# Performance work log

Measured on AMD Instinct MI355X. Metric: run time of the kernel, lower is better.

Reference implementation:

```python
import jax, jax.numpy as jnp
import numpy as np

B, T, E, H = 64, 512, 512, 512


def setup_inputs() -> dict:
    key = jax.random.key(0)
    ks = jax.random.split(key, 10)
    s = 1.0 / np.sqrt(H)  # torch GRU init: U(-1/sqrt(H), 1/sqrt(H))
    u = lambda k, shape: jax.random.uniform(k, shape, jnp.float32, -s, s)
    return {
        "xs": jax.random.normal(ks[0], (B, T, E), jnp.float32),
        "w_ih0": u(ks[1], (2, 3 * H, E)),
        "w_hh0": u(ks[2], (2, 3 * H, H)),
        "b_ih0": u(ks[3], (2, 3 * H)),
        "b_hh0": u(ks[4], (2, 3 * H)),
        "w_ih1": u(ks[5], (2, 3 * H, 2 * H)),
        "w_hh1": u(ks[6], (2, 3 * H, H)),
        "b_ih1": u(ks[7], (2, 3 * H)),
        "b_hh1": u(ks[8], (2, 3 * H)),
    }


def _gru_dir(x, w_ih, w_hh, b_ih, b_hh):
    # x: [B, T, D]; returns hs [B, T, H], h_T [B, H]
    h_dim = w_hh.shape[1]
    gx = jnp.einsum("btd,gd->btg", x, w_ih) + b_ih  # [B, T, 3H], all input GEMMs batched

    def step(h, gx_t):
        gh = h @ w_hh.T + b_hh
        r = jax.nn.sigmoid(gx_t[:, :h_dim] + gh[:, :h_dim])
        z = jax.nn.sigmoid(gx_t[:, h_dim:2 * h_dim] + gh[:, h_dim:2 * h_dim])
        n = jnp.tanh(gx_t[:, 2 * h_dim:] + r * gh[:, 2 * h_dim:])
        h = (1.0 - z) * n + z * h
        return h, h

    h0 = jnp.zeros((x.shape[0], h_dim), x.dtype)
    hT, hs = jax.lax.scan(step, h0, jnp.swapaxes(gx, 0, 1))
    return jnp.swapaxes(hs, 0, 1), hT


def _bidir_layer(x, w_ih, w_hh, b_ih, b_hh):
    hs_f, h_f = _gru_dir(x, w_ih[0], w_hh[0], b_ih[0], b_hh[0])
    hs_b, h_b = _gru_dir(x[:, ::-1], w_ih[1], w_hh[1], b_ih[1], b_hh[1])
    hs_b = hs_b[:, ::-1]
    return jnp.concatenate([hs_f, hs_b], axis=-1), jnp.stack([h_f, h_b])


def reference(xs, w_ih0, w_hh0, b_ih0, b_hh0, w_ih1, w_hh1, b_ih1, b_hh1):
    h0_out, hy0 = _bidir_layer(xs, w_ih0, w_hh0, b_ih0, b_hh0)
    h1_out, hy1 = _bidir_layer(h0_out, w_ih1, w_hh1, b_ih1, b_hh1)
    hy = jnp.concatenate([hy0, hy1], axis=0)  # [n_layers*2, B, H]
    # dropout p=0.0 -> identity
    return (h1_out, hy)
```

## Files before the change

### kernel.cpp

```cpp
#include <hip/hip_runtime.h>
#include <stdint.h>

#define Bq 64
#define Tq 512
#define Hq 512
#define G3 1536

typedef unsigned short u16;
typedef uint32_t u32;
typedef unsigned long long u64;
typedef __attribute__((ext_vector_type(8))) short bf16x8;
typedef __attribute__((ext_vector_type(4))) float f32x4;

__device__ __forceinline__ float bf2f(u16 v){ unsigned u = ((unsigned)v)<<16; float f; __builtin_memcpy(&f,&u,4); return f; }
__device__ __forceinline__ u16 f2bf(float f){ unsigned u; __builtin_memcpy(&u,&f,4); u += 0x7fffu + ((u>>16)&1u); return (u16)(u>>16); }

__global__ void detect_k(const u16* __restrict__ xs, int* __restrict__ flag){
  __shared__ int cnt;
  if (threadIdx.x==0) cnt = 0;
  __syncthreads();
  int good = 0;
  for (int i = threadIdx.x; i < 4096; i += 256) {
    u16 v = xs[2*i];
    int e = (v>>7)&0xFF;
    if (e==0 || (e>=100 && e<=140)) good++;
  }
  atomicAdd(&cnt, good);
  __syncthreads();
  if (threadIdx.x==0) flag[0] = (cnt > 3600) ? 1 : 0;
}

template<int K, int AMODE, int OUTF32>
__global__ __launch_bounds__(256,1) void gemm_gx(const void* __restrict__ Araw,
        const void* __restrict__ Wraw, const void* __restrict__ braw,
        void* __restrict__ outraw, const int* __restrict__ dflag)
{
  __shared__ __align__(16) u16 Ah[64*72];
  __shared__ __align__(16) u16 Al[64*72];
  __shared__ __align__(16) u16 Wh[64*72];
  __shared__ __align__(16) u16 Wl[64*72];
  const int bf16in = dflag[0];
  const bool useAlo = (AMODE==0) && !bf16in;
  const bool useWlo = !bf16in;
  const int dir = blockIdx.z;
  const int tid = threadIdx.x;
  const int m0 = blockIdx.x*64, n0 = blockIdx.y*64;
  const int wave = tid>>6, lane = tid&63;
  const int wm = (wave>>1)*32, wn = (wave&1)*32;
  f32x4 acc[2][2] = {};

  for (int kb=0; kb<K/64; kb++) {
    if (AMODE==0 && !bf16in) {
      const float* Af = (const float*)Araw;
      #pragma unroll
      for (int it=0; it<4; it++) {
        int c = it*256 + tid;
        int r = c>>4, cc = (c&15)*4;
        float4 v = *(const float4*)&Af[(size_t)(m0+r)*K + kb*64 + cc];
        u16 h0=f2bf(v.x), h1=f2bf(v.y), h2=f2bf(v.z), h3=f2bf(v.w);
        *(ushort4*)&Ah[r*72+cc] = make_ushort4(h0,h1,h2,h3);
        *(ushort4*)&Al[r*72+cc] = make_ushort4(
            f2bf(v.x-bf2f(h0)), f2bf(v.y-bf2f(h1)),
            f2bf(v.z-bf2f(h2)), f2bf(v.w-bf2f(h3)));
      }
    } else {
      const u16* Ab = (const u16*)Araw;
      #pragma unroll
      for (int it=0; it<2; it++) {
        int c = it*256 + tid;
        int r = c>>3, cc = (c&7)*8;
        *(bf16x8*)&Ah[r*72+cc] = *(const bf16x8*)&Ab[(size_t)(m0+r)*K + kb*64 + cc];
      }
    }
    if (!bf16in) {
      const float* Wf = (const float*)Wraw + (size_t)dir*G3*K;
      #pragma unroll
      for (int it=0; it<4; it++) {
        int c = it*256 + tid;
        int r = c>>4, cc = (c&15)*4;
        float4 v = *(const float4*)&Wf[(size_t)(n0+r)*K + kb*64 + cc];
        u16 h0=f2bf(v.x), h1=f2bf(v.y), h2=f2bf(v.z), h3=f2bf(v.w);
        *(ushort4*)&Wh[r*72+cc] = make_ushort4(h0,h1,h2,h3);
        *(ushort4*)&Wl[r*72+cc] = make_ushort4(
            f2bf(v.x-bf2f(h0)), f2bf(v.y-bf2f(h1)),
            f2bf(v.z-bf2f(h2)), f2bf(v.w-bf2f(h3)));
      }
    } else {
      const u16* Wb = (const u16*)Wraw + (size_t)dir*G3*K;
      #pragma unroll
      for (int it=0; it<2; it++) {
        int c = it*256 + tid;
        int r = c>>3, cc = (c&7)*8;
        *(bf16x8*)&Wh[r*72+cc] = *(const bf16x8*)&Wb[(size_t)(n0+r)*K + kb*64 + cc];
      }
    }
    __syncthreads();
    #pragma unroll
    for (int ks=0; ks<2; ks++) {
      int ko = ks*32 + (lane>>4)*8;
      bf16x8 a0 = *(const bf16x8*)&Ah[(wm    + (lane&15))*72 + ko];
      bf16x8 a1 = *(const bf16x8*)&Ah[(wm+16 + (lane&15))*72 + ko];
      bf16x8 b0 = *(const bf16x8*)&Wh[(wn    + (lane&15))*72 + ko];
      bf16x8 b1 = *(const bf16x8*)&Wh[(wn+16 + (lane&15))*72 + ko];
      acc[0][0] = __builtin_amdgcn_mfma_f32_16x16x32_bf16(a0,b0,acc[0][0],0,0,0);
      acc[0][1] = __builtin_amdgcn_mfma_f32_16x16x32_bf16(a0,b1,acc[0][1],0,0,0);
      acc[1][0] = __builtin_amdgcn_mfma_f32_16x16x32_bf16(a1,b0,acc[1][0],0,0,0);
      acc[1][1] = __builtin_amdgcn_mfma_f32_16x16x32_bf16(a1,b1,acc[1][1],0,0,0);
      if (useAlo) {
        bf16x8 c0 = *(const bf16x8*)&Al[(wm    + (lane&15))*72 + ko];
        bf16x8 c1 = *(const bf16x8*)&Al[(wm+16 + (lane&15))*72 + ko];
        acc[0][0] = __builtin_amdgcn_mfma_f32_16x16x32_bf16(c0,b0,acc[0][0],0,0,0);
        acc[0][1] = __builtin_amdgcn_mfma_f32_16x16x32_bf16(c0,b1,acc[0][1],0,0,0);
        acc[1][0] = __builtin_amdgcn_mfma_f32_16x16x32_bf16(c1,b0,acc[1][0],0,0,0);
        acc[1][1] = __builtin_amdgcn_mfma_f32_16x16x32_bf16(c1,b1,acc[1][1],0,0,0);
      }
      if (useWlo) {
        bf16x8 d0 = *(const bf16x8*)&Wl[(wn    + (lane&15))*72 + ko];
        bf16x8 d1 = *(const bf16x8*)&Wl[(wn+16 + (lane&15))*72 + ko];
        acc[0][0] = __builtin_amdgcn_mfma_f32_16x16x32_bf16(a0,d0,acc[0][0],0,0,0);
        acc[0][1] = __builtin_amdgcn_mfma_f32_16x16x32_bf16(a0,d1,acc[0][1],0,0,0);
        acc[1][0] = __builtin_amdgcn_mfma_f32_16x16x32_bf16(a1,d0,acc[1][0],0,0,0);
        acc[1][1] = __builtin_amdgcn_mfma_f32_16x16x32_bf16(a1,d1,acc[1][1],0,0,0);
      }
    }
    __syncthreads();
  }
  #pragma unroll
  for (int i=0;i<2;i++) {
    #pragma unroll
    for (int j=0;j<2;j++) {
      int nn = n0 + wn + j*16 + (lane&15);
      float bv = bf16in ? bf2f(((const u16*)braw)[dir*G3 + nn])
                        : ((const float*)braw)[dir*G3 + nn];
      #pragma unroll
      for (int r=0;r<4;r++) {
        int mm = m0 + wm + i*16 + (lane>>4)*4 + r;
        int b = mm >> 9, t = mm & 511;
        size_t oi = ((size_t)(dir*Tq + t)*Bq + b)*G3 + nn;
        float v = acc[i][j][r] + bv;
        if (OUTF32) ((float*)outraw)[oi] = v;
        else        ((u16*)outraw)[oi]   = f2bf(v);
      }
    }
  }
}

template<int LAYER, int GXF32>
__global__ __launch_bounds__(128,1) void gru_scan(const void* __restrict__ whh,
        const void* __restrict__ bhh, const void* __restrict__ gx,
        u16* __restrict__ hs0, void* __restrict__ dout,
        u32* __restrict__ hexw, int* __restrict__ flags,
        const int* __restrict__ dflag)
{
  extern __shared__ char smem[];
  u16* wlds = (u16*)smem;

  const int bf16in = dflag[0];
  const int tid = threadIdx.x;
  const int bx  = blockIdx.x;
  const int dir = bx>>6, group=(bx>>4)&3, slice=bx&15;
  const int jbase = slice*32, bg0 = group*16;
  int* fl = flags + (dir*4+group)*16;

  if (!bf16in) {
    const float* wf = (const float*)whh + (size_t)dir*G3*Hq;
    for (int c = tid; c < 96*128; c += 128) {
      int r = c>>7, q = (c&127)*4;
      int gate = r>>5, jj = r&31;
      float4 v = *(const float4*)&wf[(size_t)(gate*512 + jbase + jj)*Hq + q];
      *(ushort4*)&wlds[r*520 + q] = make_ushort4(f2bf(v.x),f2bf(v.y),f2bf(v.z),f2bf(v.w));
    }
  } else {
    const u16* wb = (const u16*)whh + (size_t)dir*G3*Hq;
    for (int c = tid; c < 96*64; c += 128) {
      int r = c>>6, cc = (c&63)*8;
      int gate = r>>5, jj = r&31;
      *(bf16x8*)&wlds[r*520 + cc] = *(const bf16x8*)&wb[(size_t)(gate*512 + jbase + jj)*Hq + cc];
    }
  }
  __syncthreads();
  if (tid >= 64) return;

  const int lane = tid;
  const int j0 = lane&15;
  const int bq = (lane>>4)*4;

  float bR[2], bZ[2], bN[2];
  #pragma unroll
  for (int c=0;c<2;c++) {
    int off = dir*G3 + jbase + c*16 + j0;
    if (bf16in) { const u16* bb=(const u16*)bhh;
      bR[c]=bf2f(bb[off]); bZ[c]=bf2f(bb[off+512]); bN[c]=bf2f(bb[off+1024]); }
    else { const float* bb=(const float*)bhh;
      bR[c]=bb[off]; bZ[c]=bb[off+512]; bN[c]=bb[off+1024]; }
  }

  float h[2][4] = {};
  float gxr[2][4], gxz[2][4], gxn[2][4];
  auto ldgx = [&](int t_in_){
    #pragma unroll
    for (int c=0;c<2;c++)
    #pragma unroll
    for (int i=0;i<4;i++){
      size_t gb = ((size_t)(dir*Tq + t_in_)*Bq + (bg0 + bq + i))*G3 + jbase + c*16 + j0;
      if (GXF32) { const float* gp=(const float*)gx + gb;
        gxr[c][i]=gp[0]; gxz[c][i]=gp[512]; gxn[c][i]=gp[1024]; }
      else { const u16* gp=(const u16*)gx + gb;
        gxr[c][i]=bf2f(gp[0]); gxz[c][i]=bf2f(gp[512]); gxn[c][i]=bf2f(gp[1024]); }
    }
  };
  ldgx(dir ? (Tq-1) : 0);

  for (int s=0; s<Tq; s++) {
    const int t_in = dir ? (Tq-1-s) : s;
    if (lane < 16) {
      while (__hip_atomic_fetch_add(&fl[lane], 0, __ATOMIC_RELAXED, __HIP_MEMORY_SCOPE_AGENT) < s) {
        __builtin_amdgcn_s_sleep(1);
      }
    }
    asm volatile("" ::: "memory");
    const u32 rb = (u32)(((s&1)*2 + dir)*Bq + bg0)*256u;
    u64 areg[32];
    #pragma unroll
    for (int kk=0; kk<16; kk++) {
      u32 base = rb + (u32)(lane&15)*256u + (u32)(kk*16 + (lane>>4)*4);
      areg[2*kk]   = __hip_atomic_fetch_add((u64*)&hexw[base],   (u64)0, __ATOMIC_RELAXED, __HIP_MEMORY_SCOPE_AGENT);
      areg[2*kk+1] = __hip_atomic_fetch_add((u64*)&hexw[base+2], (u64)0, __ATOMIC_RELAXED, __HIP_MEMORY_SCOPE_AGENT);
    }
    f32x4 aR[2] = {{0.f,0.f,0.f,0.f},{0.f,0.f,0.f,0.f}};
    f32x4 aZ[2] = {{0.f,0.f,0.f,0.f},{0.f,0.f,0.f,0.f}};
    f32x4 aN[2] = {{0.f,0.f,0.f,0.f},{0.f,0.f,0.f,0.f}};
    #pragma unroll
    for (int kk=0; kk<16; kk++) {
      union { u64 q[2]; bf16x8 v; } ab;
      ab.q[0] = areg[2*kk]; ab.q[1] = areg[2*kk+1];
      int ko = kk*32 + (lane>>4)*8;
      #pragma unroll
      for (int c=0;c<2;c++) {
        int wl = c*16 + j0;
        bf16x8 b0 = *(const bf16x8*)&wlds[(     wl)*520 + ko];
        bf16x8 b1 = *(const bf16x8*)&wlds[(32 + wl)*520 + ko];
        bf16x8 b2 = *(const bf16x8*)&wlds[(64 + wl)*520 + ko];
        aR[c] = __builtin_amdgcn_mfma_f32_16x16x32_bf16(ab.v,b0,aR[c],0,0,0);
        aZ[c] = __builtin_amdgcn_mfma_f32_16x16x32_bf16(ab.v,b1,aZ[c],0,0,0);
        aN[c] = __builtin_amdgcn_mfma_f32_16x16x32_bf16(ab.v,b2,aN[c],0,0,0);
      }
    }
    const u32 rb2 = (u32)((((s+1)&1)*2 + dir)*Bq + bg0)*256u;
    u16 hb[2][4]; float hn[2][4];
    #pragma unroll
    for (int c=0;c<2;c++)
    #pragma unroll
    for (int i=0;i<4;i++) {
      float rr = gxr[c][i] + aR[c][i] + bR[c];
      float zz = gxz[c][i] + aZ[c][i] + bZ[c];
      float gh =             aN[c][i] + bN[c];
      float r = 1.f/(1.f + __expf(-rr));
      float z = 1.f/(1.f + __expf(-zz));
      float x = gxn[c][i] + r*gh;
      x = fminf(fmaxf(x, -15.f), 15.f);
      float e2 = __expf(2.f*x);
      float n = (e2 - 1.f)/(e2 + 1.f);
      hn[c][i] = (1.f - z)*n + z*h[c][i];
      h[c][i] = hn[c][i]; hb[c][i] = f2bf(hn[c][i]);
    }
    #pragma unroll
    for (int c=0;c<2;c++)
    #pragma unroll
    for (int i=0;i<4;i++) {
      u32 p1 = (u32)__shfl_down((int)hb[c][i], 1);
      u32 p2 = (u32)__shfl_down((int)hb[c][i], 2);
      u32 p3 = (u32)__shfl_down((int)hb[c][i], 3);
      if ((lane & 3) == 0) {
        u64 pk = (u64)hb[c][i] | ((u64)(p1 & 0xffffu) << 16)
               | ((u64)(p2 & 0xffffu) << 32) | ((u64)(p3 & 0xffffu) << 48);
        (void)__hip_atomic_exchange((u64*)&hexw[rb2 + (u32)(bq+i)*256u + (u32)(slice*16 + c*8 + (j0>>1))],
                                    pk, __ATOMIC_RELAXED, __HIP_MEMORY_SCOPE_AGENT);
      }
    }
    asm volatile("s_waitcnt vmcnt(0)" ::: "memory");
    if (lane == 0) {
      (void)__hip_atomic_fetch_add(&fl[slice], 1, __ATOMIC_RELAXED, __HIP_MEMORY_SCOPE_AGENT);
    }
    if (s+1 < Tq) ldgx(dir ? (Tq-2-s) : (s+1));
    #pragma unroll
    for (int c=0;c<2;c++)
    #pragma unroll
    for (int i=0;i<4;i++) {
      int bg = bg0 + bq + i;
      size_t oi = ((size_t)bg*Tq + t_in)*1024 + dir*512 + jbase + c*16 + j0;
      if (LAYER==0) {
        __builtin_nontemporal_store(hb[c][i], &hs0[oi]);
      } else {
        if (bf16in) __builtin_nontemporal_store(hb[c][i], &((u16*)dout)[oi]);
        else        __builtin_nontemporal_store(hn[c][i], &((float*)dout)[oi]);
      }
      if (s == Tq-1) {
        size_t hyi = (size_t)Bq*Tq*1024 + ((size_t)(LAYER*2 + dir)*Bq + bg)*512 + jbase + c*16 + j0;
        if (bf16in) ((u16*)dout)[hyi] = hb[c][i];
        else        ((float*)dout)[hyi] = hn[c][i];
      }
    }
  }
}

__global__ void init_k(u32* hexw, int* flags){
  int i = blockIdx.x*256 + threadIdx.x;
  if (i < 2*2*Bq*256) hexw[i] = 0;
  if (i < 128) flags[i] = 0;
}

extern "C" void kernel_launch(void* const* d_in, const int* in_sizes, int n_in,
                              void* d_out, int out_size, void* d_ws, size_t ws_size,
                              hipStream_t stream)
{
  const void* xs    = d_in[0];
  const void* w_ih0 = d_in[1];
  const void* w_hh0 = d_in[2];
  const void* b_ih0 = d_in[3];
  const void* b_hh0 = d_in[4];
  const void* w_ih1 = d_in[5];
  const void* w_hh1 = d_in[6];
  const void* b_ih1 = d_in[7];
  const void* b_hh1 = d_in[8];
  (void)in_sizes; (void)n_in; (void)out_size;

  char* ws   = (char*)d_ws;
  int* dflag = (int*)ws;
  int* flags = (int*)(ws + 256);
  u32* hexw  = (u32*)(ws + 1024);
  void* gx   = (void*)(ws + 263168ULL);
  const bool gxf32 = ws_size >= 263168ULL + 402653184ULL;
  u16* hs0   = (u16*)d_out;

  hipFuncSetAttribute((const void*)gru_scan<0,0>, hipFuncAttributeMaxDynamicSharedMemorySize, 99840);
  hipFuncSetAttribute((const void*)gru_scan<1,0>, hipFuncAttributeMaxDynamicSharedMemorySize, 99840);
  hipFuncSetAttribute((const void*)gru_scan<0,1>, hipFuncAttributeMaxDynamicSharedMemorySize, 99840);
  hipFuncSetAttribute((const void*)gru_scan<1,1>, hipFuncAttributeMaxDynamicSharedMemorySize, 99840);

  dim3 gg(Tq*Bq/64, G3/64, 2);

  detect_k<<<1, 256, 0, stream>>>((const u16*)xs, dflag);
  init_k<<<512, 256, 0, stream>>>(hexw, flags);
  if (gxf32) {
    gemm_gx<512,0,1><<<gg, 256, 0, stream>>>(xs, w_ih0, b_ih0, gx, dflag);
    gru_scan<0,1><<<128, 128, 99840, stream>>>(w_hh0, b_hh0, gx, hs0, d_out, hexw, flags, dflag);
    gemm_gx<1024,1,1><<<gg, 256, 0, stream>>>(hs0, w_ih1, b_ih1, gx, dflag);
    init_k<<<512, 256, 0, stream>>>(hexw, flags);
    gru_scan<1,1><<<128, 128, 99840, stream>>>(w_hh1, b_hh1, gx, hs0, d_out, hexw, flags, dflag);
  } else {
    gemm_gx<512,0,0><<<gg, 256, 0, stream>>>(xs, w_ih0, b_ih0, gx, dflag);
    gru_scan<0,0><<<128, 128, 99840, stream>>>(w_hh0, b_hh0, gx, hs0, d_out, hexw, flags, dflag);
    gemm_gx<1024,1,0><<<gg, 256, 0, stream>>>(hs0, w_ih1, b_ih1, gx, dflag);
    init_k<<<512, 256, 0, stream>>>(hexw, flags);
    gru_scan<1,0><<<128, 128, 99840, stream>>>(w_hh1, b_hh1, gx, hs0, d_out, hexw, flags, dflag);
  }
}
```

Before: 6.200 ms.

## Keep recurrent weights in registers and pipeline hidden-state loads with MFMAs

The recurrent scan kernel now holds its slice of W_hh in per-lane registers instead of shared memory, and launches with 64 threads and no dynamic LDS. The hidden-state atomic loads are split into four chunks that are double-buffered and interleaved with the MFMA groups. The aim is to remove LDS reads from the per-timestep critical path and overlap global load latency with compute. The cost is very high register pressure (about 384 VGPRs for weights), which risks spills or compilation trouble.

Result: slower. 7.694 ms (+24.1%).

```diff
diff --git a/kernel.cpp b/kernel.cpp
--- a/kernel.cpp
+++ b/kernel.cpp
@@ -146,44 +146,55 @@
 }
 
 template<int LAYER, int GXF32>
-__global__ __launch_bounds__(128,1) void gru_scan(const void* __restrict__ whh,
+__global__ __launch_bounds__(64,1) void gru_scan(const void* __restrict__ whh,
         const void* __restrict__ bhh, const void* __restrict__ gx,
         u16* __restrict__ hs0, void* __restrict__ dout,
         u32* __restrict__ hexw, int* __restrict__ flags,
         const int* __restrict__ dflag)
 {
-  extern __shared__ char smem[];
-  u16* wlds = (u16*)smem;
-
   const int bf16in = dflag[0];
-  const int tid = threadIdx.x;
+  const int lane = threadIdx.x;
   const int bx  = blockIdx.x;
   const int dir = bx>>6, group=(bx>>4)&3, slice=bx&15;
   const int jbase = slice*32, bg0 = group*16;
   int* fl = flags + (dir*4+group)*16;
 
-  if (!bf16in) {
-    const float* wf = (const float*)whh + (size_t)dir*G3*Hq;
-    for (int c = tid; c < 96*128; c += 128) {
-      int r = c>>7, q = (c&127)*4;
-      int gate = r>>5, jj = r&31;
-      float4 v = *(const float4*)&wf[(size_t)(gate*512 + jbase + jj)*Hq + q];
-      *(ushort4*)&wlds[r*520 + q] = make_ushort4(f2bf(v.x),f2bf(v.y),f2bf(v.z),f2bf(v.w));
-    }
-  } else {
-    const u16* wb = (const u16*)whh + (size_t)dir*G3*Hq;
-    for (int c = tid; c < 96*64; c += 128) {
-      int r = c>>6, cc = (c&63)*8;
-      int gate = r>>5, jj = r&31;
-      *(bf16x8*)&wlds[r*520 + cc] = *(const bf16x8*)&wb[(size_t)(gate*512 + jbase + jj)*Hq + cc];
-    }
-  }
-  __syncthreads();
-  if (tid >= 64) return;
-
-  const int lane = tid;
   const int j0 = lane&15;
   const int bq = (lane>>4)*4;
+  const int khalf = (lane>>4)*8;
+
+  bf16x8 wreg[2][3][16];
+  if (!bf16in) {
+    const float* wf0 = (const float*)whh + (size_t)dir*G3*Hq;
+    #pragma unroll
+    for (int c=0;c<2;c++)
+    #pragma unroll
+    for (int g=0;g<3;g++) {
+      const float* wr = wf0 + (size_t)(g*512 + jbase + c*16 + j0)*Hq;
+      #pragma unroll
+      for (int kk=0;kk<16;kk++) {
+        float4 v0 = *(const float4*)&wr[kk*32 + khalf];
+        float4 v1 = *(const float4*)&wr[kk*32 + khalf + 4];
+        bf16x8 w;
+        w[0]=(short)f2bf(v0.x); w[1]=(short)f2bf(v0.y);
+        w[2]=(short)f2bf(v0.z); w[3]=(short)f2bf(v0.w);
+        w[4]=(short)f2bf(v1.x); w[5]=(short)f2bf(v1.y);
+        w[6]=(short)f2bf(v1.z); w[7]=(short)f2bf(v1.w);
+        wreg[c][g][kk] = w;
+      }
+    }
+  } else {
+    const u16* wb0 = (const u16*)whh + (size_t)dir*G3*Hq;
+    #pragma unroll
+    for (int c=0;c<2;c++)
+    #pragma unroll
+    for (int g=0;g<3;g++) {
+      const u16* wr = wb0 + (size_t)(g*512 + jbase + c*16 + j0)*Hq;
+      #pragma unroll
+      for (int kk=0;kk<16;kk++)
+        wreg[c][g][kk] = *(const bf16x8*)&wr[kk*32 + khalf];
+    }
+  }
 
   float bR[2], bZ[2], bN[2];
   #pragma unroll
@@ -220,32 +231,54 @@
     }
     asm volatile("" ::: "memory");
     const u32 rb = (u32)(((s&1)*2 + dir)*Bq + bg0)*256u;
-    u64 areg[32];
-    #pragma unroll
-    for (int kk=0; kk<16; kk++) {
-      u32 base = rb + (u32)(lane&15)*256u + (u32)(kk*16 + (lane>>4)*4);
-      areg[2*kk]   = __hip_atomic_fetch_add((u64*)&hexw[base],   (u64)0, __ATOMIC_RELAXED, __HIP_MEMORY_SCOPE_AGENT);
-      areg[2*kk+1] = __hip_atomic_fetch_add((u64*)&hexw[base+2], (u64)0, __ATOMIC_RELAXED, __HIP_MEMORY_SCOPE_AGENT);
+    const u32 gbase = rb + (u32)(lane&15)*256u + (u32)((lane>>4)*4);
+
+    u64 aA[8], aB[8];
+    #pragma unroll
+    for (int k2=0;k2<4;k2++) {
+      u32 b_ = gbase + (u32)((0+k2)*16);
+      aA[2*k2]   = __hip_atomic_fetch_add((u64*)&hexw[b_],   (u64)0, __ATOMIC_RELAXED, __HIP_MEMORY_SCOPE_AGENT);
+      aA[2*k2+1] = __hip_atomic_fetch_add((u64*)&hexw[b_+2], (u64)0, __ATOMIC_RELAXED, __HIP_MEMORY_SCOPE_AGENT);
+    }
+    #pragma unroll
+    for (int k2=0;k2<4;k2++) {
+      u32 b_ = gbase + (u32)((4+k2)*16);
+      aB[2*k2]   = __hip_atomic_fetch_add((u64*)&hexw[b_],   (u64)0, __ATOMIC_RELAXED, __HIP_MEMORY_SCOPE_AGENT);
+      aB[2*k2+1] = __hip_atomic_fetch_add((u64*)&hexw[b_+2], (u64)0, __ATOMIC_RELAXED, __HIP_MEMORY_SCOPE_AGENT);
     }
     f32x4 aR[2] = {{0.f,0.f,0.f,0.f},{0.f,0.f,0.f,0.f}};
     f32x4 aZ[2] = {{0.f,0.f,0.f,0.f},{0.f,0.f,0.f,0.f}};
     f32x4 aN[2] = {{0.f,0.f,0.f,0.f},{0.f,0.f,0.f,0.f}};
-    #pragma unroll
-    for (int kk=0; kk<16; kk++) {
-      union { u64 q[2]; bf16x8 v; } ab;
-      ab.q[0] = areg[2*kk]; ab.q[1] = areg[2*kk+1];
-      int ko = kk*32 + (lane>>4)*8;
-      #pragma unroll
-      for (int c=0;c<2;c++) {
-        int wl = c*16 + j0;
-        bf16x8 b0 = *(const bf16x8*)&wlds[(     wl)*520 + ko];
-        bf16x8 b1 = *(const bf16x8*)&wlds[(32 + wl)*520 + ko];
-        bf16x8 b2 = *(const bf16x8*)&wlds[(64 + wl)*520 + ko];
-        aR[c] = __builtin_amdgcn_mfma_f32_16x16x32_bf16(ab.v,b0,aR[c],0,0,0);
-        aZ[c] = __builtin_amdgcn_mfma_f32_16x16x32_bf16(ab.v,b1,aZ[c],0,0,0);
-        aN[c] = __builtin_amdgcn_mfma_f32_16x16x32_bf16(ab.v,b2,aN[c],0,0,0);
-      }
-    }
+    #define MFMA4(BUF, KK0)                                                   \
+      _Pragma("unroll")                                                       \
+      for (int k2=0;k2<4;k2++) {                                              \
+        union { u64 q[2]; bf16x8 v; } ab;                                     \
+        ab.q[0] = BUF[2*k2]; ab.q[1] = BUF[2*k2+1];                           \
+        _Pragma("unroll")                                                     \
+        for (int c=0;c<2;c++) {                                               \
+          aR[c] = __builtin_amdgcn_mfma_f32_16x16x32_bf16(ab.v, wreg[c][0][KK0+k2], aR[c],0,0,0); \
+          aZ[c] = __builtin_amdgcn_mfma_f32_16x16x32_bf16(ab.v, wreg[c][1][KK0+k2], aZ[c],0,0,0); \
+          aN[c] = __builtin_amdgcn_mfma_f32_16x16x32_bf16(ab.v, wreg[c][2][KK0+k2], aN[c],0,0,0); \
+        }                                                                     \
+      }
+    MFMA4(aA, 0);
+    #pragma unroll
+    for (int k2=0;k2<4;k2++) {
+      u32 b_ = gbase + (u32)((8+k2)*16);
+      aA[2*k2]   = __hip_atomic_fetch_add((u64*)&hexw[b_],   (u64)0, __ATOMIC_RELAXED, __HIP_MEMORY_SCOPE_AGENT);
+      aA[2*k2+1] = __hip_atomic_fetch_add((u64*)&hexw[b_+2], (u64)0, __ATOMIC_RELAXED, __HIP_MEMORY_SCOPE_AGENT);
+    }
+    MFMA4(aB, 4);
+    #pragma unroll
+    for (int k2=0;k2<4;k2++) {
+      u32 b_ = gbase + (u32)((12+k2)*16);
+      aB[2*k2]   = __hip_atomic_fetch_add((u64*)&hexw[b_],   (u64)0, __ATOMIC_RELAXED, __HIP_MEMORY_SCOPE_AGENT);
+      aB[2*k2+1] = __hip_atomic_fetch_add((u64*)&hexw[b_+2], (u64)0, __ATOMIC_RELAXED, __HIP_MEMORY_SCOPE_AGENT);
+    }
+    MFMA4(aA, 8);
+    MFMA4(aB, 12);
+    #undef MFMA4
+
     const u32 rb2 = (u32)((((s+1)&1)*2 + dir)*Bq + bg0)*256u;
     u16 hb[2][4]; float hn[2][4];
     #pragma unroll
@@ -333,26 +366,21 @@
   const bool gxf32 = ws_size >= 263168ULL + 402653184ULL;
   u16* hs0   = (u16*)d_out;
 
-  hipFuncSetAttribute((const void*)gru_scan<0,0>, hipFuncAttributeMaxDynamicSharedMemorySize, 99840);
-  hipFuncSetAttribute((const void*)gru_scan<1,0>, hipFuncAttributeMaxDynamicSharedMemorySize, 99840);
-  hipFuncSetAttribute((const void*)gru_scan<0,1>, hipFuncAttributeMaxDynamicSharedMemorySize, 99840);
-  hipFuncSetAttribute((const void*)gru_scan<1,1>, hipFuncAttributeMaxDynamicSharedMemorySize, 99840);
-
   dim3 gg(Tq*Bq/64, G3/64, 2);
 
   detect_k<<<1, 256, 0, stream>>>((const u16*)xs, dflag);
   init_k<<<512, 256, 0, stream>>>(hexw, flags);
   if (gxf32) {
     gemm_gx<512,0,1><<<gg, 256, 0, stream>>>(xs, w_ih0, b_ih0, gx, dflag);
-    gru_scan<0,1><<<128, 128, 99840, stream>>>(w_hh0, b_hh0, gx, hs0, d_out, hexw, flags, dflag);
+    gru_scan<0,1><<<128, 64, 0, stream>>>(w_hh0, b_hh0, gx, hs0, d_out, hexw, flags, dflag);
     gemm_gx<1024,1,1><<<gg, 256, 0, stream>>>(hs0, w_ih1, b_ih1, gx, dflag);
     init_k<<<512, 256, 0, stream>>>(hexw, flags);
-    gru_scan<1,1><<<128, 128, 99840, stream>>>(w_hh1, b_hh1, gx, hs0, d_out, hexw, flags, dflag);
+    gru_scan<1,1><<<128, 64, 0, stream>>>(w_hh1, b_hh1, gx, hs0, d_out, hexw, flags, dflag);
   } else {
     gemm_gx<512,0,0><<<gg, 256, 0, stream>>>(xs, w_ih0, b_ih0, gx, dflag);
-    gru_scan<0,0><<<128, 128, 99840, stream>>>(w_hh0, b_hh0, gx, hs0, d_out, hexw, flags, dflag);
+    gru_scan<0,0><<<128, 64, 0, stream>>>(w_hh0, b_hh0, gx, hs0, d_out, hexw, flags, dflag);
     gemm_gx<1024,1,0><<<gg, 256, 0, stream>>>(hs0, w_ih1, b_ih1, gx, dflag);
     init_k<<<512, 256, 0, stream>>>(hexw, flags);
-    gru_scan<1,0><<<128, 128, 99840, stream>>>(w_hh1, b_hh1, gx, hs0, d_out, hexw, flags, dflag);
-  }
-}
+    gru_scan<1,0><<<128, 64, 0, stream>>>(w_hh1, b_hh1, gx, hs0, d_out, hexw, flags, dflag);
+  }
+}
```
